# Kernel tuning notes

Hardware: AMD Instinct MI355X
Metric: run time of the kernel (lower is better)

Reference implementation:

```python
import jax, jax.numpy as jnp
import numpy as np

B, C, HZ, HX = 32, 256, 13, 25

# ---------- basic layers ----------

def _conv1x1(x, w, b):
    # x: [B,Cin,H,W], w: [Cout,Cin]
    return jnp.einsum('bchw,oc->bohw', x, w) + b[None, :, None, None]

def _conv2d(x, w, b, pad):
    y = jax.lax.conv_general_dilated(x, w, (1, 1), [(pad, pad), (pad, pad)],
                                     dimension_numbers=('NCHW', 'OIHW', 'NCHW'))
    return y + b[None, :, None, None]

def _bn(x, gamma, beta, mean, var):
    # eval-mode batchnorm with running stats, eps=1e-5 (torch default)
    s = gamma / jnp.sqrt(var + 1e-5)
    return x * s[None, :, None, None] + (beta - mean * s)[None, :, None, None]

def _gelu(x):
    return jax.nn.gelu(x, approximate=False)  # torch nn.GELU default = exact erf

# ---------- sparsemax (softThresholdingOperation) ----------
# The torch topk version recursively refines unresolved rows with 2*topk; since
# 2*128>=169 and 2*512>=625 it is mathematically exact sparsemax here.

def _sparsemax_impl(s):
    s = s - jnp.max(s, axis=-1, keepdims=True)
    d = s.shape[-1]
    z = -jnp.sort(-s, axis=-1)                      # descending sort
    cs = jnp.cumsum(z, axis=-1) - 1.0
    k = jnp.arange(1, d + 1, dtype=s.dtype)
    support = k * z > cs
    supp = jnp.sum(support, axis=-1, keepdims=True)  # int support size
    tau = jnp.take_along_axis(cs, supp - 1, axis=-1) / supp.astype(s.dtype)
    out = jnp.maximum(s - tau, 0.0)
    return out, (out, supp)

@jax.custom_vjp
def sparsemax(s):
    return _sparsemax_impl(s)[0]

def _sm_fwd(s):
    return _sparsemax_impl(s)

def _sm_bwd(res, g):
    out, supp = res
    gi = jnp.where(out != 0, g, 0.0)
    v_hat = jnp.sum(gi, axis=-1, keepdims=True) / supp.astype(out.dtype)
    return (jnp.where(out != 0, gi - v_hat, gi),)

sparsemax.defvjp(_sm_fwd, _sm_bwd)

# ---------- connected components + fill holes (GPU-native, no scipy) ----------

def _dilate8_max(lab):
    # 3x3 max-pool label propagation (8-connectivity, matches np.ones((3,3)))
    Bb, H, W = lab.shape
    p = jnp.pad(lab, ((0, 0), (1, 1), (1, 1)))
    shifts = [p[:, i:i + H, j:j + W] for i in range(3) for j in range(3)]
    return jnp.max(jnp.stack(shifts, 0), 0)

def _dilate4_or(x):
    # cross-shaped binary dilation (4-connectivity, scipy fill_holes default)
    Bb, H, W = x.shape
    p = jnp.pad(x, ((0, 0), (1, 1), (1, 1)))
    return (p[:, 1:H + 1, 1:W + 1] | p[:, 0:H, 1:W + 1] | p[:, 2:H + 2, 1:W + 1]
            | p[:, 1:H + 1, 0:W] | p[:, 1:H + 1, 2:W + 2])

def _largest_cc_filled(m):
    # m: bool [B,H,W] -> float mask of largest 8-connected component, holes filled
    Bb, H, W = m.shape
    HW = H * W
    idx = jnp.arange(1, HW + 1, dtype=jnp.int32).reshape(1, H, W)
    lab0 = jnp.where(m, idx, 0)

    def body(st):
        lab, _ = st
        return (jnp.where(m, _dilate8_max(lab), 0), lab)

    lab = jax.lax.while_loop(lambda st: jnp.any(st[0] != st[1]), body,
                             (lab0, -jnp.ones_like(lab0)))[0]

    counts = jax.vmap(lambda l, mm: jnp.zeros(HW + 1, jnp.int32)
                      .at[l.ravel()].add(mm.ravel()))(lab, m.astype(jnp.int32))
    largest = jnp.argmax(counts.at[:, 0].set(-1), axis=-1).astype(jnp.int32)
    comp = (lab == largest[:, None, None]) & m

    # fill holes: flood-fill background (4-conn) from the border, invert
    bg = ~comp
    border = jnp.zeros((H, W), bool).at[0].set(True).at[-1].set(True) \
        .at[:, 0].set(True).at[:, -1].set(True)
    seed = bg & border[None]

    def body2(st):
        r, _ = st
        return (bg & _dilate4_or(r), r)

    reach = jax.lax.while_loop(lambda st: jnp.any(st[0] != st[1]), body2,
                               (seed, jnp.zeros_like(seed)))[0]
    return ~reach

# ---------- module forward ----------

def _forward(zf, xf, sup_w, sup_b, sup_gamma, sup_beta, sup_mean, sup_var,
             q_w, q_b, q_gamma, q_beta, q_mean, q_var,
             g_w1, g_b1, g_w2, g_b2, g_gamma, g_beta, g_mean, g_var,
             fi_w, fi_b, fi_gamma, fi_beta, fi_mean, fi_var,
             fi1_w, fi1_b, fi1_gamma, fi1_beta, fi1_mean, fi1_var):
    Bb, Cc, Hz, Wz = zf.shape
    _, _, Hx, Wx = xf.shape

    xf_trans = _gelu(_bn(_conv1x1(xf, q_w, q_b), q_gamma, q_beta, q_mean, q_var))
    zf_trans = _gelu(_bn(_conv1x1(zf, sup_w, sup_b), sup_gamma, sup_beta, sup_mean, sup_var))
    xf_g = _gelu(_bn(_conv1x1(_conv2d(xf, g_w1, g_b1, 1), g_w2, g_b2),
                     g_gamma, g_beta, g_mean, g_var))

    zt = zf_trans.reshape(Bb, Cc, Hz * Wz)
    xt = xf_trans.reshape(Bb, Cc, Hx * Wx)
    zp = zf.reshape(Bb, Cc, Hz * Wz)
    xp = xf.reshape(Bb, Cc, Hx * Wx)

    zf_s = sparsemax(jnp.einsum('bcn,bcm->bnm', zt, zt))      # [B,169,169]
    zp = zp + jnp.einsum('bcn,bnm->bcm', zp, zf_s)

    si = sparsemax(jnp.einsum('bcn,bcm->bnm', zp, xp))         # [B,169,625]
    si2 = sparsemax(jnp.einsum('bcn,bcm->bnm', zp, xt))
    si = si + si2

    mask2 = jax.lax.stop_gradient(jnp.mean(si2, axis=1)) != 0  # [B,625]
    mask = _largest_cc_filled(mask2.reshape(Bb, Hx, Wx)).astype(xf.dtype)[:, None]

    si_img = si.reshape(Bb, Hz * Wz, Hx, Wx)                   # [B,169,25,25]
    fi_out = _gelu(_bn(_conv1x1(si_img, fi_w, fi_b), fi_gamma, fi_beta, fi_mean, fi_var))
    concat = jnp.concatenate([fi_out, xf_g * mask], axis=1)
    return _gelu(_bn(_conv2d(concat, fi1_w, fi1_b, 2),
                     fi1_gamma, fi1_beta, fi1_mean, fi1_var))

# ---------- setup ----------

def setup_inputs() -> dict:
    key = jax.random.key(0)
    ks = jax.random.split(key, 40)
    f32 = jnp.float32

    def n(k, shape, s=0.05):
        return (jax.random.normal(k, shape) * s).astype(f32)

    inp = {}
    inp['zf'] = jax.random.normal(ks[0], (B, C, HZ, HZ), f32)
    inp['xf'] = jax.random.normal(ks[1], (B, C, HX, HX), f32)

    def bn_params(pfx, k0):
        inp[pfx + '_gamma'] = (1.0 + n(ks[k0], (C,))).astype(f32)
        inp[pfx + '_beta'] = n(ks[k0 + 1], (C,))
        inp[pfx + '_mean'] = n(ks[k0 + 2], (C,))
        inp[pfx + '_var'] = jax.random.uniform(ks[k0 + 3], (C,), f32, 0.5, 1.5)

    inp['sup_w'] = n(ks[2], (C, C), 0.06); inp['sup_b'] = n(ks[3], (C,))
    bn_params('sup', 4)
    inp['q_w'] = n(ks[8], (C, C), 0.06); inp['q_b'] = n(ks[9], (C,))
    bn_params('q', 10)
    inp['g_w1'] = n(ks[14], (C, C, 3, 3), 0.02); inp['g_b1'] = n(ks[15], (C,))
    inp['g_w2'] = n(ks[16], (C, C), 0.06); inp['g_b2'] = n(ks[17], (C,))
    bn_params('g', 18)
    inp['fi_w'] = n(ks[22], (C, HZ * HZ), 0.08); inp['fi_b'] = n(ks[23], (C,))
    bn_params('fi', 24)
    inp['fi1_w'] = n(ks[28], (C, 2 * C, 5, 5), 0.01); inp['fi1_b'] = n(ks[29], (C,))
    bn_params('fi1', 30)
    return inp


def reference(zf, xf, sup_w, sup_b, sup_gamma, sup_beta, sup_mean, sup_var,
              q_w, q_b, q_gamma, q_beta, q_mean, q_var,
              g_w1, g_b1, g_w2, g_b2, g_gamma, g_beta, g_mean, g_var,
              fi_w, fi_b, fi_gamma, fi_beta, fi_mean, fi_var,
              fi1_w, fi1_b, fi1_gamma, fi1_beta, fi1_mean, fi1_var):
    return _forward(zf, xf, sup_w, sup_b, sup_gamma, sup_beta, sup_mean, sup_var,
                    q_w, q_b, q_gamma, q_beta, q_mean, q_var,
                    g_w1, g_b1, g_w2, g_b2, g_gamma, g_beta, g_mean, g_var,
                    fi_w, fi_b, fi_gamma, fi_beta, fi_mean, fi_var,
                    fi1_w, fi1_b, fi1_gamma, fi1_beta, fi1_mean, fi1_var)
```

## Files before the change

kernel.cpp:

```cpp
#include <hip/hip_runtime.h>
#include <hip/hip_bf16.h>
#include <math.h>

#define BB  32
#define CC  256
#define NZ  169
#define NX  625

typedef _Float16 f16x4 __attribute__((ext_vector_type(4)));
typedef _Float16 f16x8 __attribute__((ext_vector_type(8)));
typedef float    f32x4 __attribute__((ext_vector_type(4)));

__device__ __forceinline__ float geluf(float x) {
  return 0.5f * x * (1.0f + erff(x * 0.7071067811865476f));
}

struct GP {
  const float* A;  const float* B;
  const float* bias; const float* gamma; const float* beta; const float* mean; const float* var;
  const float* resid;
  float* out;
  int M, N, K;
  long aB, bB, outB;
};

#define TM 64
#define TN 64
#define TK 16

template<int AG, int EPI>
__global__ __launch_bounds__(256) void gemm_k(GP p) {
  const int b  = blockIdx.z;
  const int m0 = blockIdx.y * TM;
  const int n0 = blockIdx.x * TN;
  const float* Ab = p.A + (size_t)b * p.aB;
  const float* Bb = p.B + (size_t)b * p.bB;
  __shared__ __align__(16) float As[TK][TM + 4];
  __shared__ __align__(16) float Bs[TK][TN + 4];
  const int tid = threadIdx.x;
  const int tx = tid & 15, ty = tid >> 4;
  float acc[4][4] = {{0.f}};
  const int nK = (p.K + TK - 1) / TK;
  for (int kb = 0; kb < nK; ++kb) {
    const int k0 = kb * TK;
    if (AG == 0) {
      #pragma unroll
      for (int i = 0; i < 4; ++i) {
        int e = tid * 4 + i;
        int am = e >> 4, ak = e & 15;
        int gm = m0 + am, gk = k0 + ak;
        float v = 0.f;
        if (gm < p.M && gk < p.K) v = Ab[(size_t)gm * p.K + gk];
        As[ak][am] = v;
      }
    } else {
      #pragma unroll
      for (int i = 0; i < 4; ++i) {
        int e = tid + 256 * i;
        int ak = e >> 6, am = e & 63;
        int gm = m0 + am, gk = k0 + ak;
        float v = 0.f;
        if (gm < p.M && gk < p.K) v = Ab[(size_t)gk * p.M + gm];
        As[ak][am] = v;
      }
    }
    #pragma unroll
    for (int i = 0; i < 4; ++i) {
      int e = tid + 256 * i;
      int bk = e >> 6, bn = e & 63;
      int gk = k0 + bk, gn = n0 + bn;
      float v = 0.f;
      if (gk < p.K && gn < p.N) v = Bb[(size_t)gk * p.N + gn];
      Bs[bk][bn] = v;
    }
    __syncthreads();
    #pragma unroll
    for (int kk = 0; kk < TK; ++kk) {
      float av[4], bv[4];
      #pragma unroll
      for (int i2 = 0; i2 < 4; ++i2) av[i2] = As[kk][ty * 4 + i2];
      #pragma unroll
      for (int j2 = 0; j2 < 4; ++j2) bv[j2] = Bs[kk][tx * 4 + j2];
      #pragma unroll
      for (int i2 = 0; i2 < 4; ++i2)
        #pragma unroll
        for (int j2 = 0; j2 < 4; ++j2)
          acc[i2][j2] = fmaf(av[i2], bv[j2], acc[i2][j2]);
    }
    __syncthreads();
  }
  #pragma unroll
  for (int i = 0; i < 4; ++i) {
    int gm = m0 + ty * 4 + i;
    if (gm >= p.M) continue;
    float bs = 0.f, sBN = 1.f, tBN = 0.f;
    if (EPI == 2) {
      bs = p.bias[gm];
      float sc = p.gamma[gm] / sqrtf(p.var[gm] + 1e-5f);
      sBN = sc; tBN = p.beta[gm] - p.mean[gm] * sc;
    }
    #pragma unroll
    for (int j = 0; j < 4; ++j) {
      int gn = n0 + tx * 4 + j;
      if (gn >= p.N) continue;
      float v = acc[i][j];
      if (EPI == 2) { v += bs; v = v * sBN + tBN; v = geluf(v); }
      if (EPI == 3) v += p.resid[(size_t)b * p.outB + (size_t)gm * p.N + gn];
      p.out[(size_t)b * p.outB + (size_t)gm * p.N + gn] = v;
    }
  }
}

__global__ __launch_bounds__(256) void wtr_k(const float* __restrict__ W,
                                             _Float16* __restrict__ Wt,
                                             int M, int C2, int C2p, int R) {
  size_t o = (size_t)blockIdx.x * 256 + threadIdx.x;
  size_t total = (size_t)R * M * C2p;
  if (o >= total) return;
  int c = (int)(o % C2p);
  int t = (int)(o / C2p);
  int m = t % M;
  int r = t / M;
  float v = 0.f;
  if (c < C2) v = W[((size_t)m * C2 + c) * R + r];
  Wt[o] = (_Float16)v;
}

__global__ __launch_bounds__(256) void cvt_k(const float* __restrict__ A,
                                             const float* __restrict__ A2,
                                             _Float16* __restrict__ O,
                                             int C, int Cp, long total) {
  long o = (long)blockIdx.x * 256 + threadIdx.x;
  if (o >= total) return;
  int c = (int)(o % Cp);
  long t = o / Cp;
  int pp = (int)(t % NX);
  int b = (int)(t / NX);
  float v = 0.f;
  if (c < C) {
    size_t src = ((size_t)b * C + c) * NX + pp;
    v = A[src];
    if (A2) v += A2[src];
  }
  O[o] = (_Float16)v;
}

struct MP {
  const _Float16* Wt;
  const _Float16* U;
  const float* mask;
  const float* bias; const float* gamma; const float* beta; const float* mean; const float* var;
  float* out;
  _Float16* out16;
  int R, Rw, C2p;
  long uB;
  int oC2p, oCoff;
};

template<int EPI, int OUT16, int MASKED>
__global__ __launch_bounds__(256) void mgemm_k(MP p) {
  const int L   = blockIdx.x + 10 * (blockIdx.y + 2 * blockIdx.z);
  const int xcd = L & 7;
  const int j   = L >> 3;
  const int jb  = j / 20;
  const int b   = (xcd << 2) + jb;
  const int t   = j - jb * 20;
  const int ty2 = t / 10;
  const int m0  = ty2 * 128;
  const int n0  = (t - ty2 * 10) * 64;

  __shared__ __align__(16) _Float16 As[128][64];
  __shared__ __align__(16) _Float16 Bs[64][64];
  const int tid = threadIdx.x;
  const int w = tid >> 6, lane = tid & 63;
  const int lm = lane & 15, q = lane >> 4;
  const int am = tid >> 1, ah = tid & 1;
  const int bn = tid >> 2, bs4 = (tid & 3);
  const int bc = bs4 * 16;
  const int ng = n0 + bn;
  const bool nv = ng < NX;
  const int py = ng / 25, px = ng - (ng / 25) * 25;
  const _Float16* Ub = p.U + (size_t)b * p.uB;
  const float* mb = MASKED ? (p.mask + (size_t)b * NX) : nullptr;
  const int pad = p.Rw >> 1;

  f32x4 acc[2][4] = {};

  for (int r = 0; r < p.R; ++r) {
    const int kh = r / p.Rw, kw = r - (r / p.Rw) * p.Rw;
    const int iy = py + kh - pad, ix = px + kw - pad;
    const bool pv = nv && ((unsigned)iy < 25u) && ((unsigned)ix < 25u);
    const int pp = iy * 25 + ix;
    const _Float16* Up = pv ? (Ub + (size_t)pp * p.C2p) : nullptr;
    _Float16 mh = (_Float16)1.f;
    if (MASKED && pv) mh = (_Float16)mb[pp];
    const _Float16* Wr = p.Wt + ((size_t)r * 256 + m0) * p.C2p;
    for (int c0 = 0; c0 < p.C2p; c0 += 64) {
      const _Float16* Arow = Wr + (size_t)am * p.C2p + c0 + ah * 32;
      f16x8 a0 = *(const f16x8*)(Arow);
      f16x8 a1 = *(const f16x8*)(Arow + 8);
      f16x8 a2 = *(const f16x8*)(Arow + 16);
      f16x8 a3 = *(const f16x8*)(Arow + 24);
      f16x8 v0 = {}, v1 = {};
      if (pv) {
        const _Float16* Bp = Up + c0 + bc;
        v0 = *(const f16x8*)(Bp);
        v1 = *(const f16x8*)(Bp + 8);
        if (MASKED && (c0 + bc) >= 256) { v0 = v0 * mh; v1 = v1 * mh; }
      }
      {
        const int ar7 = am & 7, abase = ah * 4;
        *(f16x8*)&As[am][((abase + 0) ^ ar7) << 3] = a0;
        *(f16x8*)&As[am][((abase + 1) ^ ar7) << 3] = a1;
        *(f16x8*)&As[am][((abase + 2) ^ ar7) << 3] = a2;
        *(f16x8*)&As[am][((abase + 3) ^ ar7) << 3] = a3;
        const int br7 = bn & 7, bbase = bs4 * 2;
        *(f16x8*)&Bs[bn][((bbase + 0) ^ br7) << 3] = v0;
        *(f16x8*)&Bs[bn][((bbase + 1) ^ br7) << 3] = v1;
      }
      __syncthreads();
      #pragma unroll
      for (int ks = 0; ks < 2; ++ks) {
        const int so = (((ks << 2) + q) ^ (lm & 7)) << 3;
        f16x8 af[2], bf[4];
        #pragma unroll
        for (int fm = 0; fm < 2; ++fm)
          af[fm] = *(const f16x8*)&As[w * 32 + fm * 16 + lm][so];
        #pragma unroll
        for (int fn = 0; fn < 4; ++fn)
          bf[fn] = *(const f16x8*)&Bs[fn * 16 + lm][so];
        #pragma unroll
        for (int fm = 0; fm < 2; ++fm)
          #pragma unroll
          for (int fn = 0; fn < 4; ++fn)
            acc[fm][fn] = __builtin_amdgcn_mfma_f32_16x16x32_f16(
                af[fm], bf[fn], acc[fm][fn], 0, 0, 0);
      }
      __syncthreads();
    }
  }
  #pragma unroll
  for (int fm = 0; fm < 2; ++fm) {
    const int rbase = m0 + w * 32 + fm * 16 + q * 4;
    #pragma unroll
    for (int rr = 0; rr < 4; ++rr) {
      const int row = rbase + rr;
      float bs = p.bias[row];
      float sBN = 1.f, tBN = 0.f;
      if (EPI == 2) {
        float sc = p.gamma[row] / sqrtf(p.var[row] + 1e-5f);
        sBN = sc; tBN = p.beta[row] - p.mean[row] * sc;
      }
      #pragma unroll
      for (int fn = 0; fn < 4; ++fn) {
        const int col = n0 + fn * 16 + lm;
        if (col < NX) {
          float v = acc[fm][fn][rr] + bs;
          if (EPI == 2) v = geluf(v * sBN + tBN);
          if (OUT16) {
            p.out16[((size_t)b * NX + col) * p.oC2p + p.oCoff + row] = (_Float16)v;
          } else {
            p.out[(size_t)b * (256 * NX) + (size_t)row * NX + col] = v;
          }
        }
      }
    }
  }
}

__global__ __launch_bounds__(256) void sparsemax_k(float* __restrict__ S, int d) {
  const int row = blockIdx.x;
  float* s = S + (size_t)row * d;
  const int tid = threadIdx.x;
  const int wid = tid >> 6, lane = tid & 63;
  float v[3]; bool act[3];
  #pragma unroll
  for (int j = 0; j < 3; ++j) {
    int idx = tid + j * 256;
    bool ok = idx < d;
    v[j] = ok ? s[idx] : -1e30f;
    act[j] = ok;
  }
  __shared__ float red[16];
  float mx = fmaxf(fmaxf(v[0], v[1]), v[2]);
  #pragma unroll
  for (int o = 32; o; o >>= 1) mx = fmaxf(mx, __shfl_down(mx, o));
  if (lane == 0) red[wid] = mx;
  __syncthreads();
  if (tid == 0) red[0] = fmaxf(fmaxf(red[0], red[1]), fmaxf(red[2], red[3]));
  __syncthreads();
  mx = red[0];
  __syncthreads();
  #pragma unroll
  for (int j = 0; j < 3; ++j) if (act[j]) v[j] -= mx;
  float tau = 0.f;
  for (int it = 0; it < 700; ++it) {
    float ls = 0.f, lc = 0.f;
    #pragma unroll
    for (int j = 0; j < 3; ++j) if (act[j]) { ls += v[j]; lc += 1.f; }
    #pragma unroll
    for (int o = 32; o; o >>= 1) { ls += __shfl_down(ls, o); lc += __shfl_down(lc, o); }
    if (lane == 0) { red[wid] = ls; red[4 + wid] = lc; }
    __syncthreads();
    if (tid == 0) {
      float Sm = 0.f, Cn = 0.f;
      #pragma unroll
      for (int w2 = 0; w2 < 4; ++w2) { Sm += red[w2]; Cn += red[4 + w2]; }
      red[8] = (Sm - 1.f) / Cn;
      red[9] = 0.f;
    }
    __syncthreads();
    tau = red[8];
    bool ch = false;
    #pragma unroll
    for (int j = 0; j < 3; ++j)
      if (act[j] && v[j] <= tau) { act[j] = false; ch = true; }
    if (ch) red[9] = 1.f;
    __syncthreads();
    if (red[9] == 0.f) break;
  }
  #pragma unroll
  for (int j = 0; j < 3; ++j) {
    int idx = tid + j * 256;
    if (idx < d) s[idx] = fmaxf(v[j] - tau, 0.f);
  }
}

__global__ __launch_bounds__(640) void cc_kernel(const float* __restrict__ si2,
                                                 float* __restrict__ mask) {
  const int b = blockIdx.x, tid = threadIdx.x;
  __shared__ int lab[625];
  __shared__ int counts[626];
  __shared__ int flag, best;
  const bool in = tid < 625;
  const int y = tid / 25, x = tid - (tid / 25) * 25;
  bool mv = false;
  if (in) {
    const float* base = si2 + (size_t)b * NZ * NX + tid;
    for (int n = 0; n < NZ; ++n) mv = mv || (base[(size_t)n * NX] > 0.f);
    lab[tid] = mv ? tid + 1 : 0;
  }
  __syncthreads();
  for (int it = 0; it < 1000; ++it) {
    if (tid == 0) flag = 0;
    __syncthreads();
    int nl = 0;
    if (in && mv) {
      nl = lab[tid];
      #pragma unroll
      for (int dy = -1; dy <= 1; ++dy)
        #pragma unroll
        for (int dx = -1; dx <= 1; ++dx) {
          int yy = y + dy, xx = x + dx;
          if ((unsigned)yy < 25u && (unsigned)xx < 25u) nl = max(nl, lab[yy * 25 + xx]);
        }
    }
    __syncthreads();
    if (in && mv && nl != lab[tid]) { lab[tid] = nl; flag = 1; }
    __syncthreads();
    if (flag == 0) break;
  }
  if (tid < 626) counts[tid] = (tid == 0) ? -1 : 0;
  if (tid == 0) best = (int)0x80000000;
  __syncthreads();
  if (in && mv) atomicAdd(&counts[lab[tid]], 1);
  __syncthreads();
  if (tid < 626) atomicMax(&best, counts[tid] * 1024 + (1023 - tid));
  __syncthreads();
  const int largest = 1023 - (best & 1023);
  const bool comp = in && mv && (lab[tid] == largest);
  const bool bg = in && !comp;
  const bool border = in && (y == 0 || y == 24 || x == 0 || x == 24);
  __syncthreads();
  if (in) lab[tid] = (bg && border) ? 1 : 0;
  __syncthreads();
  for (int it = 0; it < 1000; ++it) {
    if (tid == 0) flag = 0;
    __syncthreads();
    int r = 0;
    if (in && bg && !lab[tid]) {
      if (y > 0  && lab[tid - 25]) r = 1;
      if (y < 24 && lab[tid + 25]) r = 1;
      if (x > 0  && lab[tid - 1])  r = 1;
      if (x < 24 && lab[tid + 1])  r = 1;
    }
    __syncthreads();
    if (r) { lab[tid] = 1; flag = 1; }
    __syncthreads();
    if (flag == 0) break;
  }
  if (in) mask[(size_t)b * NX + tid] = lab[tid] ? 0.f : 1.f;
}

extern "C" void kernel_launch(void* const* d_in, const int* in_sizes, int n_in,
                              void* d_out, int out_size, void* d_ws, size_t ws_size,
                              hipStream_t stream) {
  const float* zf     = (const float*)d_in[0];
  const float* xf     = (const float*)d_in[1];
  const float* sup_w  = (const float*)d_in[2];
  const float* sup_b  = (const float*)d_in[3];
  const float* sup_g  = (const float*)d_in[4];
  const float* sup_be = (const float*)d_in[5];
  const float* sup_m  = (const float*)d_in[6];
  const float* sup_v  = (const float*)d_in[7];
  const float* q_w    = (const float*)d_in[8];
  const float* q_b    = (const float*)d_in[9];
  const float* q_g    = (const float*)d_in[10];
  const float* q_be   = (const float*)d_in[11];
  const float* q_m    = (const float*)d_in[12];
  const float* q_v    = (const float*)d_in[13];
  const float* g_w1   = (const float*)d_in[14];
  const float* g_b1   = (const float*)d_in[15];
  const float* g_w2   = (const float*)d_in[16];
  const float* g_b2   = (const float*)d_in[17];
  const float* g_g    = (const float*)d_in[18];
  const float* g_be   = (const float*)d_in[19];
  const float* g_m    = (const float*)d_in[20];
  const float* g_v    = (const float*)d_in[21];
  const float* fi_w   = (const float*)d_in[22];
  const float* fi_b   = (const float*)d_in[23];
  const float* fi_g   = (const float*)d_in[24];
  const float* fi_be  = (const float*)d_in[25];
  const float* fi_m   = (const float*)d_in[26];
  const float* fi_v   = (const float*)d_in[27];
  const float* fi1_w  = (const float*)d_in[28];
  const float* fi1_b  = (const float*)d_in[29];
  const float* fi1_g  = (const float*)d_in[30];
  const float* fi1_be = (const float*)d_in[31];
  const float* fi1_m  = (const float*)d_in[32];
  const float* fi1_v  = (const float*)d_in[33];

  float* ws = (float*)d_ws;
  float* xf_trans = ws;
  float* zf_trans = xf_trans + 5120000;
  float* zf_s     = zf_trans + 1384448;
  float* zp2      = zf_s + 913952;
  float* si       = zp2 + 1384448;
  float* si2      = si + 3380000;
  float* maskb    = si2 + 3380000;
  float* tail     = maskb + 20000;

  _Float16* xf16 = (_Float16*)tail;
  _Float16* gt16 = xf16 + 5120000;
  _Float16* Ucat = gt16 + 5120000;
  _Float16* S16  = Ucat + 10240000;

  _Float16* wt_g1  = (_Float16*)xf_trans;
  _Float16* wt_g2  = wt_g1 + 589824;
  _Float16* wt_fi  = wt_g2 + 65536;
  _Float16* wt_fi1 = wt_fi + 49152;

  dim3 blk(256);
  GP p;

  p = GP{}; p.A = q_w; p.B = xf; p.bias = q_b;
  p.gamma = q_g; p.beta = q_be; p.mean = q_m; p.var = q_v;
  p.out = xf_trans; p.M = CC; p.N = NX; p.K = CC;
  p.aB = 0; p.bB = (long)CC * NX; p.outB = (long)CC * NX;
  gemm_k<0,2><<<dim3(10,4,BB), blk, 0, stream>>>(p);

  p = GP{}; p.A = sup_w; p.B = zf; p.bias = sup_b;
  p.gamma = sup_g; p.beta = sup_be; p.mean = sup_m; p.var = sup_v;
  p.out = zf_trans; p.M = CC; p.N = NZ; p.K = CC;
  p.aB = 0; p.bB = (long)CC * NZ; p.outB = (long)CC * NZ;
  gemm_k<0,2><<<dim3(3,4,BB), blk, 0, stream>>>(p);

  p = GP{}; p.A = zf_trans; p.B = zf_trans;
  p.out = zf_s; p.M = NZ; p.N = NZ; p.K = CC;
  p.aB = (long)CC * NZ; p.bB = (long)CC * NZ; p.outB = (long)NZ * NZ;
  gemm_k<1,0><<<dim3(3,3,BB), blk, 0, stream>>>(p);

  sparsemax_k<<<BB * NZ, blk, 0, stream>>>(zf_s, NZ);

  p = GP{}; p.A = zf; p.B = zf_s; p.resid = zf;
  p.out = zp2; p.M = CC; p.N = NZ; p.K = NZ;
  p.aB = (long)CC * NZ; p.bB = (long)NZ * NZ; p.outB = (long)CC * NZ;
  gemm_k<0,3><<<dim3(3,4,BB), blk, 0, stream>>>(p);

  p = GP{}; p.A = zp2; p.B = xf;
  p.out = si; p.M = NZ; p.N = NX; p.K = CC;
  p.aB = (long)CC * NZ; p.bB = (long)CC * NX; p.outB = (long)NZ * NX;
  gemm_k<1,0><<<dim3(10,3,BB), blk, 0, stream>>>(p);

  p = GP{}; p.A = zp2; p.B = xf_trans;
  p.out = si2; p.M = NZ; p.N = NX; p.K = CC;
  p.aB = (long)CC * NZ; p.bB = (long)CC * NX; p.outB = (long)NZ * NX;
  gemm_k<1,0><<<dim3(10,3,BB), blk, 0, stream>>>(p);

  sparsemax_k<<<BB * NZ, blk, 0, stream>>>(si, NX);
  sparsemax_k<<<BB * NZ, blk, 0, stream>>>(si2, NX);

  cc_kernel<<<BB, dim3(640), 0, stream>>>(si2, maskb);

  wtr_k<<<(9*256*256 + 255)/256,  blk, 0, stream>>>(g_w1,  wt_g1,  256, 256, 256, 9);
  wtr_k<<<(256*256   + 255)/256,  blk, 0, stream>>>(g_w2,  wt_g2,  256, 256, 256, 1);
  wtr_k<<<(256*192   + 255)/256,  blk, 0, stream>>>(fi_w,  wt_fi,  256, 169, 192, 1);
  wtr_k<<<(25*256*512+ 255)/256,  blk, 0, stream>>>(fi1_w, wt_fi1, 256, 512, 512, 25);

  cvt_k<<<(long)(BB*NX*256 + 255)/256, blk, 0, stream>>>(xf, nullptr, xf16, 256, 256, (long)BB*NX*256);
  cvt_k<<<(long)(BB*NX*192 + 255)/256, blk, 0, stream>>>(si, si2, S16, 169, 192, (long)BB*NX*192);

  MP mp;

  mp = MP{}; mp.Wt = wt_g1; mp.U = xf16; mp.bias = g_b1;
  mp.out16 = gt16; mp.R = 9; mp.Rw = 3; mp.C2p = 256;
  mp.uB = (long)NX * 256; mp.oC2p = 256; mp.oCoff = 0;
  mgemm_k<1,1,0><<<dim3(10,2,BB), blk, 0, stream>>>(mp);

  mp = MP{}; mp.Wt = wt_g2; mp.U = gt16; mp.bias = g_b2;
  mp.gamma = g_g; mp.beta = g_be; mp.mean = g_m; mp.var = g_v;
  mp.out16 = Ucat; mp.R = 1; mp.Rw = 1; mp.C2p = 256;
  mp.uB = (long)NX * 256; mp.oC2p = 512; mp.oCoff = 256;
  mgemm_k<2,1,0><<<dim3(10,2,BB), blk, 0, stream>>>(mp);

  mp = MP{}; mp.Wt = wt_fi; mp.U = S16; mp.bias = fi_b;
  mp.gamma = fi_g; mp.beta = fi_be; mp.mean = fi_m; mp.var = fi_v;
  mp.out16 = Ucat; mp.R = 1; mp.Rw = 1; mp.C2p = 192;
  mp.uB = (long)NX * 192; mp.oC2p = 512; mp.oCoff = 0;
  mgemm_k<2,1,0><<<dim3(10,2,BB), blk, 0, stream>>>(mp);

  mp = MP{}; mp.Wt = wt_fi1; mp.U = Ucat; mp.mask = maskb;
  mp.bias = fi1_b; mp.gamma = fi1_g; mp.beta = fi1_be; mp.mean = fi1_m; mp.var = fi1_v;
  mp.out = (float*)d_out; mp.R = 25; mp.Rw = 5; mp.C2p = 512;
  mp.uB = (long)NX * 512;
  mgemm_k<2,0,1><<<dim3(10,2,BB), blk, 0, stream>>>(mp);
}
```

Measured before the change: 889.0 us.

## Prefetch conv-GEMM tiles into registers and read weights directly, merge sparsemax launches

The implicit-GEMM conv kernel now loads each wave's weight fragments straight from global memory into registers in MFMA layout, so the weight tile no longer goes through LDS. The loop over taps and channel chunks becomes one flattened loop that prefetches the next weight and activation tiles into registers while the current MFMAs run. This hides global-load latency and cuts LDS traffic and one barrier per step, at the cost of more registers and uncoalesced per-wave weight reads. Separately, the two sparsemax launches become one launch over twice as many rows, which is only correct if si2 sits directly after si in memory.

```diff
diff --git a/kernel.cpp b/kernel.cpp
--- a/kernel.cpp
+++ b/kernel.cpp
@@ -169,75 +169,102 @@
   const int m0  = ty2 * 128;
   const int n0  = (t - ty2 * 10) * 64;
 
-  __shared__ __align__(16) _Float16 As[128][64];
   __shared__ __align__(16) _Float16 Bs[64][64];
   const int tid = threadIdx.x;
   const int w = tid >> 6, lane = tid & 63;
   const int lm = lane & 15, q = lane >> 4;
-  const int am = tid >> 1, ah = tid & 1;
   const int bn = tid >> 2, bs4 = (tid & 3);
   const int bc = bs4 * 16;
+  const int br7 = bn & 7, bbase = bs4 * 2;
   const int ng = n0 + bn;
   const bool nv = ng < NX;
   const int py = ng / 25, px = ng - (ng / 25) * 25;
   const _Float16* Ub = p.U + (size_t)b * p.uB;
   const float* mb = MASKED ? (p.mask + (size_t)b * NX) : nullptr;
   const int pad = p.Rw >> 1;
+  const int nC = p.C2p >> 6;
+  const int KT = p.R * nC;
+  const size_t tapStride = (size_t)256 * p.C2p;
+  const _Float16* Abase = p.Wt + (size_t)(m0 + w * 32 + lm) * p.C2p + q * 8;
 
   f32x4 acc[2][4] = {};
 
-  for (int r = 0; r < p.R; ++r) {
-    const int kh = r / p.Rw, kw = r - (r / p.Rw) * p.Rw;
-    const int iy = py + kh - pad, ix = px + kw - pad;
-    const bool pv = nv && ((unsigned)iy < 25u) && ((unsigned)ix < 25u);
-    const int pp = iy * 25 + ix;
-    const _Float16* Up = pv ? (Ub + (size_t)pp * p.C2p) : nullptr;
-    _Float16 mh = (_Float16)1.f;
-    if (MASKED && pv) mh = (_Float16)mb[pp];
-    const _Float16* Wr = p.Wt + ((size_t)r * 256 + m0) * p.C2p;
-    for (int c0 = 0; c0 < p.C2p; c0 += 64) {
-      const _Float16* Arow = Wr + (size_t)am * p.C2p + c0 + ah * 32;
-      f16x8 a0 = *(const f16x8*)(Arow);
-      f16x8 a1 = *(const f16x8*)(Arow + 8);
-      f16x8 a2 = *(const f16x8*)(Arow + 16);
-      f16x8 a3 = *(const f16x8*)(Arow + 24);
-      f16x8 v0 = {}, v1 = {};
-      if (pv) {
-        const _Float16* Bp = Up + c0 + bc;
-        v0 = *(const f16x8*)(Bp);
-        v1 = *(const f16x8*)(Bp + 8);
-        if (MASKED && (c0 + bc) >= 256) { v0 = v0 * mh; v1 = v1 * mh; }
+  int r = 0, ci = 0, kh = 0, kw = 0;
+  int iy = py - pad, ix = px - pad;
+  bool pv = nv && ((unsigned)iy < 25u) && ((unsigned)ix < 25u);
+  int pp = iy * 25 + ix;
+  _Float16 mh = (_Float16)1.f;
+  if (MASKED && pv) mh = (_Float16)mb[pp];
+
+  f16x8 Brg0 = {}, Brg1 = {};
+  if (pv) {
+    const _Float16* Bp = Ub + (size_t)pp * p.C2p + bc;
+    Brg0 = *(const f16x8*)(Bp);
+    Brg1 = *(const f16x8*)(Bp + 8);
+    if (MASKED && bc >= 256) { Brg0 = Brg0 * mh; Brg1 = Brg1 * mh; }
+  }
+  f16x8 Acur[2][2], Anxt[2][2];
+  #pragma unroll
+  for (int fm = 0; fm < 2; ++fm)
+    #pragma unroll
+    for (int ks = 0; ks < 2; ++ks)
+      Acur[fm][ks] = *(const f16x8*)(Abase + (size_t)fm * 16 * p.C2p + ks * 32);
+
+  for (int kt = 0; kt < KT; ++kt) {
+    int ci_n = ci + 1, r_n = r, kh_n = kh, kw_n = kw;
+    if (ci_n == nC) {
+      ci_n = 0; r_n = r + 1;
+      kw_n = kw + 1; if (kw_n == p.Rw) { kw_n = 0; kh_n = kh + 1; }
+    }
+    *(f16x8*)&Bs[bn][((bbase + 0) ^ br7) << 3] = Brg0;
+    *(f16x8*)&Bs[bn][((bbase + 1) ^ br7) << 3] = Brg1;
+    __syncthreads();
+    bool pv_n = pv; int pp_n = pp; _Float16 mh_n = mh;
+    if (kt + 1 < KT) {
+      if (r_n != r) {
+        int iy2 = py + kh_n - pad, ix2 = px + kw_n - pad;
+        pv_n = nv && ((unsigned)iy2 < 25u) && ((unsigned)ix2 < 25u);
+        pp_n = iy2 * 25 + ix2;
+        mh_n = (_Float16)1.f;
+        if (MASKED && pv_n) mh_n = (_Float16)mb[pp_n];
       }
-      {
-        const int ar7 = am & 7, abase = ah * 4;
-        *(f16x8*)&As[am][((abase + 0) ^ ar7) << 3] = a0;
-        *(f16x8*)&As[am][((abase + 1) ^ ar7) << 3] = a1;
-        *(f16x8*)&As[am][((abase + 2) ^ ar7) << 3] = a2;
-        *(f16x8*)&As[am][((abase + 3) ^ ar7) << 3] = a3;
-        const int br7 = bn & 7, bbase = bs4 * 2;
-        *(f16x8*)&Bs[bn][((bbase + 0) ^ br7) << 3] = v0;
-        *(f16x8*)&Bs[bn][((bbase + 1) ^ br7) << 3] = v1;
+      f16x8 nb0 = {}, nb1 = {};
+      if (pv_n) {
+        const _Float16* Bp = Ub + (size_t)pp_n * p.C2p + ci_n * 64 + bc;
+        nb0 = *(const f16x8*)(Bp);
+        nb1 = *(const f16x8*)(Bp + 8);
+        if (MASKED && (ci_n * 64 + bc) >= 256) { nb0 = nb0 * mh_n; nb1 = nb1 * mh_n; }
       }
-      __syncthreads();
-      #pragma unroll
-      for (int ks = 0; ks < 2; ++ks) {
-        const int so = (((ks << 2) + q) ^ (lm & 7)) << 3;
-        f16x8 af[2], bf[4];
+      Brg0 = nb0; Brg1 = nb1;
+      const _Float16* An = Abase + (size_t)r_n * tapStride + ci_n * 64;
+      #pragma unroll
+      for (int fm = 0; fm < 2; ++fm)
         #pragma unroll
-        for (int fm = 0; fm < 2; ++fm)
-          af[fm] = *(const f16x8*)&As[w * 32 + fm * 16 + lm][so];
+        for (int ks = 0; ks < 2; ++ks)
+          Anxt[fm][ks] = *(const f16x8*)(An + (size_t)fm * 16 * p.C2p + ks * 32);
+    }
+    #pragma unroll
+    for (int ks = 0; ks < 2; ++ks) {
+      const int so = (((ks << 2) + q) ^ (lm & 7)) << 3;
+      f16x8 bf[4];
+      #pragma unroll
+      for (int fn = 0; fn < 4; ++fn)
+        bf[fn] = *(const f16x8*)&Bs[fn * 16 + lm][so];
+      #pragma unroll
+      for (int fm = 0; fm < 2; ++fm)
         #pragma unroll
         for (int fn = 0; fn < 4; ++fn)
-          bf[fn] = *(const f16x8*)&Bs[fn * 16 + lm][so];
-        #pragma unroll
-        for (int fm = 0; fm < 2; ++fm)
-          #pragma unroll
-          for (int fn = 0; fn < 4; ++fn)
-            acc[fm][fn] = __builtin_amdgcn_mfma_f32_16x16x32_f16(
-                af[fm], bf[fn], acc[fm][fn], 0, 0, 0);
-      }
-      __syncthreads();
-    }
+          acc[fm][fn] = __builtin_amdgcn_mfma_f32_16x16x32_f16(
+              Acur[fm][ks], bf[fn], acc[fm][fn], 0, 0, 0);
+    }
+    __syncthreads();
+    #pragma unroll
+    for (int fm = 0; fm < 2; ++fm)
+      #pragma unroll
+      for (int ks = 0; ks < 2; ++ks)
+        Acur[fm][ks] = Anxt[fm][ks];
+    pv = pv_n; pp = pp_n; mh = mh_n;
+    r = r_n; ci = ci_n; kh = kh_n; kw = kw_n;
   }
   #pragma unroll
   for (int fm = 0; fm < 2; ++fm) {
@@ -487,8 +514,7 @@
   p.aB = (long)CC * NZ; p.bB = (long)CC * NX; p.outB = (long)NZ * NX;
   gemm_k<1,0><<<dim3(10,3,BB), blk, 0, stream>>>(p);
 
-  sparsemax_k<<<BB * NZ, blk, 0, stream>>>(si, NX);
-  sparsemax_k<<<BB * NZ, blk, 0, stream>>>(si2, NX);
+  sparsemax_k<<<2 * BB * NZ, blk, 0, stream>>>(si, NX);
 
   cc_kernel<<<BB, dim3(640), 0, stream>>>(si2, maskb);
 
```

After: 991.6 us. 1.12x slower.
